# Performance work log

Measured on AMD Instinct MI355X. Metric: run time of the kernel, lower is better.

## Reference

```python
import jax, jax.numpy as jnp
import numpy as np

N_NODES = 50000
N_EDGES = 600000
D = 128
N_LAYERS = 4  # 2 base + 2 resnet layers
N_GRAPHS = 64
NEG_SLOPE = 0.01  # F.leaky_relu default


def setup_inputs() -> dict:
    key = jax.random.key(0)
    k1, k2, k3, k4, k5 = jax.random.split(key, 5)
    x = jax.random.normal(k1, (N_NODES, D), dtype=jnp.float32)
    edge_index = jax.random.randint(k2, (2, N_EDGES), 0, N_NODES, dtype=jnp.int64)
    batch = jnp.sort(jax.random.randint(k3, (N_NODES,), 0, N_GRAPHS, dtype=jnp.int64))
    Wl = jax.random.normal(k4, (N_LAYERS, D, D), dtype=jnp.float32) * 0.05
    bl = jnp.zeros((N_LAYERS, D), dtype=jnp.float32)
    Wr = jax.random.normal(k5, (N_LAYERS, D, D), dtype=jnp.float32) * 0.05
    return {"x": x, "edge_index": edge_index, "batch": batch,
            "Wl": Wl, "bl": bl, "Wr": Wr}


def _mean_aggregate(x, src, dst, n_nodes):
    # mean over incoming neighbors; isolated nodes get 0 (PyG scatter-mean semantics)
    s = jax.ops.segment_sum(x[src], dst, num_segments=n_nodes)  # [N, D]
    cnt = jax.ops.segment_sum(jnp.ones((src.shape[0],), x.dtype), dst,
                              num_segments=n_nodes)
    return s / jnp.maximum(cnt, 1.0)[:, None]


def reference(x, edge_index, batch, Wl, bl, Wr):
    src, dst = edge_index[0], edge_index[1]
    n = x.shape[0]
    for i in range(N_LAYERS):
        agg = _mean_aggregate(x, src, dst, n)                      # [N, D]
        # SAGEConv: lin_l(agg) + lin_r(x); lin_l has bias, lin_r does not
        x_new = agg @ Wl[i].T + bl[i] + x @ Wr[i].T
        x_new = jnp.where(x_new >= 0, x_new, NEG_SLOPE * x_new)    # leaky_relu
        x = x_new if i < 2 else x + x_new                          # residual after first 2
    # global mean pool per graph
    pooled = jax.ops.segment_sum(x, batch, num_segments=N_GRAPHS)  # [G, D]
    counts = jax.ops.segment_sum(jnp.ones((n,), x.dtype), batch,
                                 num_segments=N_GRAPHS)
    return pooled / jnp.maximum(counts, 1.0)[:, None]
```

## Files before the change

### kernel.cpp

```cpp
#include <hip/hip_runtime.h>

#define N_NODES 50000
#define N_EDGES 600000
#define DIM 128
#define N_LAYERS 4
#define N_GRAPHS 64
#define NEG_SLOPE 0.01f
#define NB_SCAN ((N_NODES + 255) / 256)
#define NB_CNT ((N_EDGES + 255) / 256)
#define NC_CONV (N_NODES * DIM / 8 / 256)
#define NB_PACK 64
#define RS 264

typedef __attribute__((ext_vector_type(8))) short short8;
typedef __attribute__((ext_vector_type(16))) float floatx16;

__device__ __forceinline__ unsigned short f2bf(float f) {
    union { float f; unsigned u; } c; c.f = f;
    unsigned u = c.u;
    unsigned r = (u + 0x7FFFu + ((u >> 16) & 1u)) >> 16;
    return (unsigned short)r;
}
__device__ __forceinline__ float bfraw2f(unsigned short b) {
    union { unsigned u; float f; } c; c.u = ((unsigned)b) << 16;
    return c.f;
}
__device__ __forceinline__ float bflo(unsigned u) {
    union { unsigned u; float f; } c; c.u = u << 16; return c.f;
}
__device__ __forceinline__ float bfhi(unsigned u) {
    union { unsigned u; float f; } c; c.u = u & 0xFFFF0000u; return c.f;
}

__global__ void zero2(int* a, int na, int* b, int nb) {
    int i = blockIdx.x * blockDim.x + threadIdx.x;
    if (i < na) a[i] = 0;
    else if (i < na + nb) b[i - na] = 0;
}

__global__ void preprocess(const float4* __restrict__ x, uint4* __restrict__ xb,
                           const float* __restrict__ Wl, const float* __restrict__ Wr,
                           ushort* __restrict__ wpk,
                           const int* __restrict__ edst, int* __restrict__ deg) {
    int b = blockIdx.x;
    if (b < NC_CONV) {
        int i = b * 256 + threadIdx.x;
        float4 a = x[i * 2], c = x[i * 2 + 1];
        uint4 o;
        o.x = ((unsigned)f2bf(a.y) << 16) | f2bf(a.x);
        o.y = ((unsigned)f2bf(a.w) << 16) | f2bf(a.z);
        o.z = ((unsigned)f2bf(c.y) << 16) | f2bf(c.x);
        o.w = ((unsigned)f2bf(c.w) << 16) | f2bf(c.z);
        xb[i] = o;
    } else if (b < NC_CONV + NB_PACK) {
        int u = (b - NC_CONV) * 4 + (threadIdx.x >> 6);
        int l = threadIdx.x & 63;
        int layer = u >> 6, m = (u >> 5) & 1, s = (u >> 2) & 7, tt = u & 3;
        const float* W = ((m == 0) ? Wl : Wr) + (size_t)layer * DIM * DIM;
        int n = tt * 32 + (l & 31);
        int kb = s * 16 + (l >> 5) * 8;
        size_t off = ((size_t)u * 64 + l) * 8;
        for (int j = 0; j < 8; j++)
            wpk[off + j] = f2bf(W[n * DIM + kb + j]);
    } else {
        int e = (b - NC_CONV - NB_PACK) * 256 + threadIdx.x;
        if (e < N_EDGES) atomicAdd(&deg[edst[e]], 1);
    }
}

__global__ void scan_pass1(const int* __restrict__ deg, int* __restrict__ bsum) {
    int i = blockIdx.x * 256 + threadIdx.x;
    int v = (i < N_NODES) ? deg[i] : 0;
    for (int off = 32; off > 0; off >>= 1) v += __shfl_down(v, off, 64);
    __shared__ int ws[4];
    int lane = threadIdx.x & 63, w = threadIdx.x >> 6;
    if (lane == 0) ws[w] = v;
    __syncthreads();
    if (threadIdx.x == 0) bsum[blockIdx.x] = ws[0] + ws[1] + ws[2] + ws[3];
}

__global__ void scan_pass2(int* __restrict__ bsum) {
    __shared__ int sm[256];
    int t = threadIdx.x;
    int v = (t < NB_SCAN) ? bsum[t] : 0;
    sm[t] = v;
    __syncthreads();
    for (int off = 1; off < 256; off <<= 1) {
        int u = (t >= off) ? sm[t - off] : 0;
        __syncthreads();
        sm[t] += u;
        __syncthreads();
    }
    if (t < NB_SCAN) bsum[t] = sm[t] - v;
}

__global__ void scan_pass3(const int* __restrict__ deg, const int* __restrict__ bsum,
                           int* __restrict__ rp) {
    int i = blockIdx.x * 256 + threadIdx.x;
    int v = (i < N_NODES) ? deg[i] : 0;
    int lane = threadIdx.x & 63, w = threadIdx.x >> 6;
    int s = v;
    for (int off = 1; off < 64; off <<= 1) {
        int t = __shfl_up(s, off, 64);
        if (lane >= off) s += t;
    }
    __shared__ int ws[4];
    if (lane == 63) ws[w] = s;
    __syncthreads();
    int wo = 0;
    for (int k = 0; k < 4; k++) wo += (k < w) ? ws[k] : 0;
    int incl = s + wo + bsum[blockIdx.x];
    if (i < N_NODES) rp[i + 1] = incl;
    if (i == 0) rp[0] = 0;
}

__global__ void fill_gstart(const int* __restrict__ src, const int* __restrict__ dst,
                            const int* __restrict__ rp, int* __restrict__ fill,
                            int* __restrict__ csr,
                            const int* __restrict__ batch, int* __restrict__ gstart) {
    int b = blockIdx.x;
    if (b < NB_CNT) {
        int e = b * 256 + threadIdx.x;
        if (e >= N_EDGES) return;
        int d = dst[e];
        int pos = atomicAdd(&fill[d], 1);
        csr[rp[d] + pos] = src[e];
    } else {
        int i = (b - NB_CNT) * 256 + threadIdx.x;
        if (i >= N_NODES) return;
        int g0 = batch[i];
        if (i == 0) {
            for (int g = 0; g <= g0; g++) gstart[g] = 0;
        } else {
            int p = batch[i - 1];
            for (int g = p + 1; g <= g0; g++) gstart[g] = i;
        }
        if (i == N_NODES - 1) {
            for (int g = g0 + 1; g <= N_GRAPHS; g++) gstart[g] = N_NODES;
        }
    }
}

__global__ __launch_bounds__(256) void agg_mean_wave4(const uint4* __restrict__ x16B,
                                                      const int* __restrict__ rp,
                                                      const int* __restrict__ csr,
                                                      uint4* __restrict__ agg16B) {
    int wv = threadIdx.x >> 6, lane = threadIdx.x & 63;
    int node = blockIdx.x * 4 + wv;
    if (node >= N_NODES) return;
    int s = rp[node], e = rp[node + 1];
    int ll = lane & 15, eg = lane >> 4;
    float a0 = 0.f, a1 = 0.f, a2 = 0.f, a3 = 0.f, a4 = 0.f, a5 = 0.f, a6 = 0.f, a7 = 0.f;
    for (int base = s; base < e; base += 64) {
        int cnt = min(64, e - base);
        unsigned myidx = (base + lane < e) ? (unsigned)csr[base + lane] : 0u;
        for (int j = 0; j < cnt; j += 16) {
            uint4 v[4];
#pragma unroll
            for (int k = 0; k < 4; k++) {
                int sel = j + k * 4 + eg;
                unsigned idx = __shfl(myidx, sel, 64);
                v[k] = make_uint4(0u, 0u, 0u, 0u);
                if (sel < cnt) v[k] = x16B[(size_t)idx * 16 + ll];
            }
#pragma unroll
            for (int k = 0; k < 4; k++) {
                a0 += bflo(v[k].x); a1 += bfhi(v[k].x);
                a2 += bflo(v[k].y); a3 += bfhi(v[k].y);
                a4 += bflo(v[k].z); a5 += bfhi(v[k].z);
                a6 += bflo(v[k].w); a7 += bfhi(v[k].w);
            }
        }
    }
    a0 += __shfl_xor(a0, 16, 64); a0 += __shfl_xor(a0, 32, 64);
    a1 += __shfl_xor(a1, 16, 64); a1 += __shfl_xor(a1, 32, 64);
    a2 += __shfl_xor(a2, 16, 64); a2 += __shfl_xor(a2, 32, 64);
    a3 += __shfl_xor(a3, 16, 64); a3 += __shfl_xor(a3, 32, 64);
    a4 += __shfl_xor(a4, 16, 64); a4 += __shfl_xor(a4, 32, 64);
    a5 += __shfl_xor(a5, 16, 64); a5 += __shfl_xor(a5, 32, 64);
    a6 += __shfl_xor(a6, 16, 64); a6 += __shfl_xor(a6, 32, 64);
    a7 += __shfl_xor(a7, 16, 64); a7 += __shfl_xor(a7, 32, 64);
    if (eg == 0) {
        float inv = 1.0f / (float)max(e - s, 1);
        uint4 o;
        o.x = ((unsigned)f2bf(a1 * inv) << 16) | f2bf(a0 * inv);
        o.y = ((unsigned)f2bf(a3 * inv) << 16) | f2bf(a2 * inv);
        o.z = ((unsigned)f2bf(a5 * inv) << 16) | f2bf(a4 * inv);
        o.w = ((unsigned)f2bf(a7 * inv) << 16) | f2bf(a6 * inv);
        agg16B[(size_t)node * 16 + ll] = o;
    }
}

__global__ __launch_bounds__(256, 4) void fused_layer_mfma(const ushort* __restrict__ agg,
                                                           const ushort* __restrict__ xin,
                                                           ushort* __restrict__ xout,
                                                           const ushort* __restrict__ wpk,
                                                           const float* __restrict__ bias,
                                                           int residual) {
    __shared__ ushort sA[64 * RS];
    int t = threadIdx.x;
    int node0 = blockIdx.x * 64;

    const uint4* aggv = (const uint4*)(agg + (size_t)node0 * DIM);
    const uint4* xv   = (const uint4*)(xin + (size_t)node0 * DIM);
    for (int i = t; i < 64 * 32; i += 256) {
        int r = i >> 5, c = i & 31;
        uint4 val = make_uint4(0u, 0u, 0u, 0u);
        if (node0 + r < N_NODES)
            val = (c < 16) ? aggv[r * 16 + c] : xv[r * 16 + (c - 16)];
        *(uint4*)&sA[r * RS + c * 8] = val;
    }
    __syncthreads();

    int w = t >> 6, l = t & 63;
    int m0 = (w >> 1) * 32;
    int th = w & 1;
    const ushort* arow = &sA[(m0 + (l & 31)) * RS];
    int khalf = (l >> 5) * 8;

    floatx16 acc0, acc1;
    for (int ii = 0; ii < 16; ii++) acc0[ii] = acc1[ii] = 0.f;

    const ushort* wl8 = wpk + (size_t)l * 8 + (size_t)(2 * th) * 512;
#pragma unroll
    for (int s2 = 0; s2 < 16; s2++) {
        int m = s2 >> 3, s = s2 & 7;
        short8 a = *(const short8*)(arow + m * 128 + s * 16 + khalf);
        size_t fb = (size_t)((m * 8 + s) * 4) * 512;
        short8 b0 = *(const short8*)(wl8 + fb);
        short8 b1 = *(const short8*)(wl8 + fb + 512);
        acc0 = __builtin_amdgcn_mfma_f32_32x32x16_bf16(a, b0, acc0, 0, 0, 0);
        acc1 = __builtin_amdgcn_mfma_f32_32x32x16_bf16(a, b1, acc1, 0, 0, 0);
    }

    int col = l & 31;
    int rbase = 4 * (l >> 5);
    floatx16 accs[2] = {acc0, acc1};
    for (int ti = 0; ti < 2; ti++) {
        int n = (2 * th + ti) * 32 + col;
        float bv = bias[n];
#pragma unroll
        for (int r = 0; r < 16; r++) {
            int row = (r & 3) + 8 * (r >> 2) + rbase;
            int gm = m0 + row;
            int gn = node0 + gm;
            if (gn >= N_NODES) continue;
            float v = accs[ti][r] + bv;
            v = (v >= 0.f) ? v : NEG_SLOPE * v;
            if (residual) v += bfraw2f(sA[gm * RS + 128 + n]);
            xout[(size_t)gn * DIM + n] = f2bf(v);
        }
    }
}

__global__ __launch_bounds__(128) void pool_partial(const ushort* __restrict__ xb,
                                                    const int* __restrict__ batch,
                                                    float* __restrict__ pooled) {
    int nb = blockIdx.x * 128;
    int ne = min(nb + 128, N_NODES);
    int d = threadIdx.x;
    int gcur = batch[nb];
    float acc = 0.f;
    for (int n = nb; n < ne; n++) {
        int g = batch[n];
        if (g != gcur) {
            atomicAdd(&pooled[gcur * DIM + d], acc);
            acc = 0.f;
            gcur = g;
        }
        acc += bfraw2f(xb[(size_t)n * DIM + d]);
    }
    atomicAdd(&pooled[gcur * DIM + d], acc);
}

__global__ void pool_final(const float* __restrict__ pooled,
                           const int* __restrict__ gstart,
                           float* __restrict__ out) {
    int i = blockIdx.x * blockDim.x + threadIdx.x;
    if (i >= N_GRAPHS * DIM) return;
    int g = i >> 7;
    int cnt = gstart[g + 1] - gstart[g];
    out[i] = pooled[i] / (float)max(cnt, 1);
}


extern "C" void kernel_launch(void* const* d_in, const int* in_sizes, int n_in,
                              void* d_out, int out_size, void* d_ws, size_t ws_size,
                              hipStream_t stream) {
    const float* x     = (const float*)d_in[0];
    const int*   ei    = (const int*)d_in[1];
    const int*   batch = (const int*)d_in[2];
    const float* Wl    = (const float*)d_in[3];
    const float* bl    = (const float*)d_in[4];
    const float* Wr    = (const float*)d_in[5];
    float* out = (float*)d_out;

    const int* esrc = ei;
    const int* edst = ei + N_EDGES;

    ushort* xb0  = (ushort*)d_ws;
    ushort* xbuf = xb0 + (size_t)N_NODES * DIM;
    ushort* agg  = xbuf + (size_t)N_NODES * DIM;
    ushort* wpk  = agg + (size_t)N_NODES * DIM;
    int* deg    = (int*)(wpk + (size_t)N_LAYERS * 2 * DIM * DIM);
    int* fill   = deg + N_NODES;
    int* csr    = fill + N_NODES;
    int* rp     = csr + N_EDGES;
    int* gstart = rp + (N_NODES + 1);
    int* bsum   = gstart + (N_GRAPHS + 1);
    float* pooled = (float*)(bsum + NB_SCAN);

    zero2<<<(2 * N_NODES + N_GRAPHS * DIM + 255) / 256, 256, 0, stream>>>(
        deg, 2 * N_NODES, (int*)pooled, N_GRAPHS * DIM);

    preprocess<<<NC_CONV + NB_PACK + NB_CNT, 256, 0, stream>>>(
        (const float4*)x, (uint4*)xb0, Wl, Wr, wpk, edst, deg);

    scan_pass1<<<NB_SCAN, 256, 0, stream>>>(deg, bsum);
    scan_pass2<<<1, 256, 0, stream>>>(bsum);
    scan_pass3<<<NB_SCAN, 256, 0, stream>>>(deg, bsum, rp);

    fill_gstart<<<NB_CNT + NB_SCAN, 256, 0, stream>>>(esrc, edst, rp, fill, csr,
                                                      batch, gstart);

    int agg_blocks = (N_NODES + 3) / 4;
    int gemm_blocks = (N_NODES + 63) / 64;
    for (int l = 0; l < N_LAYERS; l++) {
        const ushort* xin = (l == 0) ? xb0 : xbuf;
        agg_mean_wave4<<<agg_blocks, 256, 0, stream>>>((const uint4*)xin, rp, csr, (uint4*)agg);
        fused_layer_mfma<<<gemm_blocks, 256, 0, stream>>>(
            agg, xin, xbuf, wpk + (size_t)l * 2 * DIM * DIM,
            bl + (size_t)l * DIM, (l >= 2) ? 1 : 0);
    }

    pool_partial<<<(N_NODES + 127) / 128, 128, 0, stream>>>(xbuf, batch, pooled);
    pool_final<<<(N_GRAPHS * DIM + 255) / 256, 256, 0, stream>>>(pooled, gstart, out);
}
```

Before: 337.7 us.

## Fuse neighbor mean aggregation and final pooling into the MFMA layer kernel

The separate aggregation kernel is removed. Each wave of the layer kernel now gathers and averages neighbor rows for 16 nodes and writes the bf16 mean straight into shared memory beside the self features. This removes the global write and re-read of the aggregate buffer and one launch per layer. Input and output buffers now ping-pong, because neighbor rows are read while new rows are written. The last layer skips writing node features and accumulates global-mean-pool partial sums with atomics, replacing the separate pool kernel. The trade-off is that each wave handles its nodes one after another, with far fewer waves in flight than the old one-wave-per-node gather, so gather latency may be hidden less well.

```diff
diff --git a/kernel.cpp b/kernel.cpp
--- a/kernel.cpp
+++ b/kernel.cpp
@@ -141,78 +141,79 @@
     }
 }
 
-__global__ __launch_bounds__(256) void agg_mean_wave4(const uint4* __restrict__ x16B,
-                                                      const int* __restrict__ rp,
-                                                      const int* __restrict__ csr,
-                                                      uint4* __restrict__ agg16B) {
-    int wv = threadIdx.x >> 6, lane = threadIdx.x & 63;
-    int node = blockIdx.x * 4 + wv;
-    if (node >= N_NODES) return;
-    int s = rp[node], e = rp[node + 1];
-    int ll = lane & 15, eg = lane >> 4;
-    float a0 = 0.f, a1 = 0.f, a2 = 0.f, a3 = 0.f, a4 = 0.f, a5 = 0.f, a6 = 0.f, a7 = 0.f;
-    for (int base = s; base < e; base += 64) {
-        int cnt = min(64, e - base);
-        unsigned myidx = (base + lane < e) ? (unsigned)csr[base + lane] : 0u;
-        for (int j = 0; j < cnt; j += 16) {
-            uint4 v[4];
-#pragma unroll
-            for (int k = 0; k < 4; k++) {
-                int sel = j + k * 4 + eg;
-                unsigned idx = __shfl(myidx, sel, 64);
-                v[k] = make_uint4(0u, 0u, 0u, 0u);
-                if (sel < cnt) v[k] = x16B[(size_t)idx * 16 + ll];
-            }
-#pragma unroll
-            for (int k = 0; k < 4; k++) {
-                a0 += bflo(v[k].x); a1 += bfhi(v[k].x);
-                a2 += bflo(v[k].y); a3 += bfhi(v[k].y);
-                a4 += bflo(v[k].z); a5 += bfhi(v[k].z);
-                a6 += bflo(v[k].w); a7 += bfhi(v[k].w);
-            }
-        }
-    }
-    a0 += __shfl_xor(a0, 16, 64); a0 += __shfl_xor(a0, 32, 64);
-    a1 += __shfl_xor(a1, 16, 64); a1 += __shfl_xor(a1, 32, 64);
-    a2 += __shfl_xor(a2, 16, 64); a2 += __shfl_xor(a2, 32, 64);
-    a3 += __shfl_xor(a3, 16, 64); a3 += __shfl_xor(a3, 32, 64);
-    a4 += __shfl_xor(a4, 16, 64); a4 += __shfl_xor(a4, 32, 64);
-    a5 += __shfl_xor(a5, 16, 64); a5 += __shfl_xor(a5, 32, 64);
-    a6 += __shfl_xor(a6, 16, 64); a6 += __shfl_xor(a6, 32, 64);
-    a7 += __shfl_xor(a7, 16, 64); a7 += __shfl_xor(a7, 32, 64);
-    if (eg == 0) {
-        float inv = 1.0f / (float)max(e - s, 1);
-        uint4 o;
-        o.x = ((unsigned)f2bf(a1 * inv) << 16) | f2bf(a0 * inv);
-        o.y = ((unsigned)f2bf(a3 * inv) << 16) | f2bf(a2 * inv);
-        o.z = ((unsigned)f2bf(a5 * inv) << 16) | f2bf(a4 * inv);
-        o.w = ((unsigned)f2bf(a7 * inv) << 16) | f2bf(a6 * inv);
-        agg16B[(size_t)node * 16 + ll] = o;
-    }
-}
-
-__global__ __launch_bounds__(256, 4) void fused_layer_mfma(const ushort* __restrict__ agg,
-                                                           const ushort* __restrict__ xin,
-                                                           ushort* __restrict__ xout,
-                                                           const ushort* __restrict__ wpk,
-                                                           const float* __restrict__ bias,
-                                                           int residual) {
+__global__ __launch_bounds__(256, 4) void fused_layer_mfma(
+    const ushort* __restrict__ xin, ushort* __restrict__ xout,
+    const int* __restrict__ rp, const int* __restrict__ csr,
+    const ushort* __restrict__ wpk, const float* __restrict__ bias,
+    const int* __restrict__ batch, float* __restrict__ pooled,
+    int residual, int do_pool) {
     __shared__ ushort sA[64 * RS];
     int t = threadIdx.x;
     int node0 = blockIdx.x * 64;
-
-    const uint4* aggv = (const uint4*)(agg + (size_t)node0 * DIM);
-    const uint4* xv   = (const uint4*)(xin + (size_t)node0 * DIM);
-    for (int i = t; i < 64 * 32; i += 256) {
-        int r = i >> 5, c = i & 31;
+    int w = t >> 6, l = t & 63;
+
+    const uint4* xv = (const uint4*)(xin + (size_t)node0 * DIM);
+#pragma unroll
+    for (int i = 0; i < 4; i++) {
+        int idx = t + i * 256;
+        int r = idx >> 4, c = idx & 15;
         uint4 val = make_uint4(0u, 0u, 0u, 0u);
-        if (node0 + r < N_NODES)
-            val = (c < 16) ? aggv[r * 16 + c] : xv[r * 16 + (c - 16)];
-        *(uint4*)&sA[r * RS + c * 8] = val;
+        if (node0 + r < N_NODES) val = xv[r * 16 + c];
+        *(uint4*)&sA[r * RS + 128 + c * 8] = val;
+    }
+
+    {
+        int ll = l & 15, eg = l >> 4;
+        int nb = node0 + w * 16;
+        int rpv = rp[min(nb + l, N_NODES)];
+        const uint4* x16B = (const uint4*)xin;
+        for (int i = 0; i < 16; i++) {
+            int s = __shfl(rpv, i, 64);
+            int e = __shfl(rpv, i + 1, 64);
+            float a0 = 0.f, a1 = 0.f, a2 = 0.f, a3 = 0.f,
+                  a4 = 0.f, a5 = 0.f, a6 = 0.f, a7 = 0.f;
+            for (int base = s; base < e; base += 64) {
+                int cnt = min(64, e - base);
+                unsigned myidx = (base + l < e) ? (unsigned)csr[base + l] : 0u;
+                for (int j = 0; j < cnt; j += 16) {
+                    uint4 v[4];
+#pragma unroll
+                    for (int k = 0; k < 4; k++) {
+                        int sel = j + k * 4 + eg;
+                        unsigned idx = __shfl(myidx, sel, 64);
+                        v[k] = make_uint4(0u, 0u, 0u, 0u);
+                        if (sel < cnt) v[k] = x16B[(size_t)idx * 16 + ll];
+                    }
+#pragma unroll
+                    for (int k = 0; k < 4; k++) {
+                        a0 += bflo(v[k].x); a1 += bfhi(v[k].x);
+                        a2 += bflo(v[k].y); a3 += bfhi(v[k].y);
+                        a4 += bflo(v[k].z); a5 += bfhi(v[k].z);
+                        a6 += bflo(v[k].w); a7 += bfhi(v[k].w);
+                    }
+                }
+            }
+            a0 += __shfl_xor(a0, 16, 64); a0 += __shfl_xor(a0, 32, 64);
+            a1 += __shfl_xor(a1, 16, 64); a1 += __shfl_xor(a1, 32, 64);
+            a2 += __shfl_xor(a2, 16, 64); a2 += __shfl_xor(a2, 32, 64);
+            a3 += __shfl_xor(a3, 16, 64); a3 += __shfl_xor(a3, 32, 64);
+            a4 += __shfl_xor(a4, 16, 64); a4 += __shfl_xor(a4, 32, 64);
+            a5 += __shfl_xor(a5, 16, 64); a5 += __shfl_xor(a5, 32, 64);
+            a6 += __shfl_xor(a6, 16, 64); a6 += __shfl_xor(a6, 32, 64);
+            a7 += __shfl_xor(a7, 16, 64); a7 += __shfl_xor(a7, 32, 64);
+            if (eg == 0) {
+                float inv = 1.0f / (float)max(e - s, 1);
+                uint4 o;
+                o.x = ((unsigned)f2bf(a1 * inv) << 16) | f2bf(a0 * inv);
+                o.y = ((unsigned)f2bf(a3 * inv) << 16) | f2bf(a2 * inv);
+                o.z = ((unsigned)f2bf(a5 * inv) << 16) | f2bf(a4 * inv);
+                o.w = ((unsigned)f2bf(a7 * inv) << 16) | f2bf(a6 * inv);
+                *(uint4*)&sA[(w * 16 + i) * RS + ll * 8] = o;
+            }
+        }
     }
     __syncthreads();
 
-    int w = t >> 6, l = t & 63;
     int m0 = (w >> 1) * 32;
     int th = w & 1;
     const ushort* arow = &sA[(m0 + (l & 31)) * RS];
@@ -236,41 +237,49 @@
     int col = l & 31;
     int rbase = 4 * (l >> 5);
     floatx16 accs[2] = {acc0, acc1};
-    for (int ti = 0; ti < 2; ti++) {
-        int n = (2 * th + ti) * 32 + col;
-        float bv = bias[n];
-#pragma unroll
-        for (int r = 0; r < 16; r++) {
-            int row = (r & 3) + 8 * (r >> 2) + rbase;
-            int gm = m0 + row;
-            int gn = node0 + gm;
-            if (gn >= N_NODES) continue;
-            float v = accs[ti][r] + bv;
-            v = (v >= 0.f) ? v : NEG_SLOPE * v;
-            if (residual) v += bfraw2f(sA[gm * RS + 128 + n]);
-            xout[(size_t)gn * DIM + n] = f2bf(v);
-        }
-    }
-}
-
-__global__ __launch_bounds__(128) void pool_partial(const ushort* __restrict__ xb,
-                                                    const int* __restrict__ batch,
-                                                    float* __restrict__ pooled) {
-    int nb = blockIdx.x * 128;
-    int ne = min(nb + 128, N_NODES);
-    int d = threadIdx.x;
-    int gcur = batch[nb];
-    float acc = 0.f;
-    for (int n = nb; n < ne; n++) {
-        int g = batch[n];
-        if (g != gcur) {
-            atomicAdd(&pooled[gcur * DIM + d], acc);
-            acc = 0.f;
-            gcur = g;
-        }
-        acc += bfraw2f(xb[(size_t)n * DIM + d]);
-    }
-    atomicAdd(&pooled[gcur * DIM + d], acc);
+    if (!do_pool) {
+#pragma unroll
+        for (int ti = 0; ti < 2; ti++) {
+            int n = (2 * th + ti) * 32 + col;
+            float bv = bias[n];
+#pragma unroll
+            for (int r = 0; r < 16; r++) {
+                int row = (r & 3) + 8 * (r >> 2) + rbase;
+                int gm = m0 + row;
+                int gn = node0 + gm;
+                if (gn >= N_NODES) continue;
+                float v = accs[ti][r] + bv;
+                v = (v >= 0.f) ? v : NEG_SLOPE * v;
+                if (residual) v += bfraw2f(sA[gm * RS + 128 + n]);
+                xout[(size_t)gn * DIM + n] = f2bf(v);
+            }
+        }
+    } else {
+        bool fast = (node0 + 63 < N_NODES) && (batch[node0] == batch[node0 + 63]);
+        int g0 = batch[node0];
+#pragma unroll
+        for (int ti = 0; ti < 2; ti++) {
+            int n = (2 * th + ti) * 32 + col;
+            float bv = bias[n];
+            float psum = 0.f;
+#pragma unroll
+            for (int r = 0; r < 16; r++) {
+                int row = (r & 3) + 8 * (r >> 2) + rbase;
+                int gm = m0 + row;
+                int gn = node0 + gm;
+                if (gn >= N_NODES) continue;
+                float v = accs[ti][r] + bv;
+                v = (v >= 0.f) ? v : NEG_SLOPE * v;
+                if (residual) v += bfraw2f(sA[gm * RS + 128 + n]);
+                if (fast) psum += v;
+                else atomicAdd(&pooled[batch[gn] * DIM + n], v);
+            }
+            if (fast) {
+                psum += __shfl_xor(psum, 32, 64);
+                if (l < 32) atomicAdd(&pooled[g0 * DIM + n], psum);
+            }
+        }
+    }
 }
 
 __global__ void pool_final(const float* __restrict__ pooled,
@@ -323,16 +332,16 @@
     fill_gstart<<<NB_CNT + NB_SCAN, 256, 0, stream>>>(esrc, edst, rp, fill, csr,
                                                       batch, gstart);
 
-    int agg_blocks = (N_NODES + 3) / 4;
     int gemm_blocks = (N_NODES + 63) / 64;
+    const ushort* xi = xb0;
+    ushort* xo = xbuf;
     for (int l = 0; l < N_LAYERS; l++) {
-        const ushort* xin = (l == 0) ? xb0 : xbuf;
-        agg_mean_wave4<<<agg_blocks, 256, 0, stream>>>((const uint4*)xin, rp, csr, (uint4*)agg);
         fused_layer_mfma<<<gemm_blocks, 256, 0, stream>>>(
-            agg, xin, xbuf, wpk + (size_t)l * 2 * DIM * DIM,
-            bl + (size_t)l * DIM, (l >= 2) ? 1 : 0);
-    }
-
-    pool_partial<<<(N_NODES + 127) / 128, 128, 0, stream>>>(xbuf, batch, pooled);
+            xi, xo, rp, csr, wpk + (size_t)l * 2 * DIM * DIM,
+            bl + (size_t)l * DIM, batch, pooled,
+            (l >= 2) ? 1 : 0, (l == N_LAYERS - 1) ? 1 : 0);
+        ushort* tmp = (ushort*)xi; xi = xo; xo = tmp;
+    }
+
     pool_final<<<(N_GRAPHS * DIM + 255) / 256, 256, 0, stream>>>(pooled, gstart, out);
 }
```

Result: faster. 325.3 us (-3.7%).
